# Kernel tuning notes

Measured on AMD Instinct MI355X. Metric: run time of the kernel, lower is better.

The kernel has to match this reference:

```python
import jax, jax.numpy as jnp
import numpy as np

N_NODES = 500000


def _gconv(x, src, dst, ew, w_neigh, b, w_self):
    # DGL GraphConv(norm='none'): multiply weight first (in>=out here), then aggregate.
    h = x @ w_neigh                      # [N, out]
    msg = h[src] * ew[:, None]           # [E, out]
    agg = jax.ops.segment_sum(msg, dst, num_segments=N_NODES)
    return agg + b + x @ w_self          # neigh conv (+bias) + self-loop linear (no bias)


def setup_inputs() -> dict:
    key = jax.random.key(0)
    ks = jax.random.split(key, 16)
    N, E, G, F = N_NODES, 16000000, 64, 16
    inp = {
        "x": jax.random.normal(ks[0], (N, F), jnp.float32),
        "src": jax.random.randint(ks[1], (E,), 0, N),
        "dst": jax.random.randint(ks[2], (E,), 0, N),
        "graph_id": jnp.sort(jax.random.randint(ks[3], (N,), 0, G)),
        "edge_weight": jax.random.uniform(ks[4], (E,), jnp.float32),
        "num_graphs": G,
        "w_neigh0": jax.random.normal(ks[5], (F, 1), jnp.float32),
        "b0": jax.random.normal(ks[6], (1,), jnp.float32),
        "w_self0": jax.random.normal(ks[7], (F, 1), jnp.float32),
        "w_neigh1": jax.random.normal(ks[8], (1, 1), jnp.float32),
        "b1": jax.random.normal(ks[9], (1,), jnp.float32),
        "w_self1": jax.random.normal(ks[10], (1, 1), jnp.float32),
        "w_neigh2": jax.random.normal(ks[11], (1, 1), jnp.float32),
        "b2": jax.random.normal(ks[12], (1,), jnp.float32),
        "w_self2": jax.random.normal(ks[13], (1, 1), jnp.float32),
        "fc1_w": jax.random.normal(ks[14], (8, 1), jnp.float32),
        "fc1_b": jax.random.normal(ks[15], (8,), jnp.float32),
        "out_w": jax.random.normal(jax.random.fold_in(key, 100), (4, 8), jnp.float32),
        "out_b": jax.random.normal(jax.random.fold_in(key, 101), (4,), jnp.float32),
    }
    return inp


def reference(x, src, dst, graph_id, edge_weight, num_graphs,
              w_neigh0, b0, w_self0, w_neigh1, b1, w_self1,
              w_neigh2, b2, w_self2, fc1_w, fc1_b, out_w, out_b):
    h = jax.nn.relu(_gconv(x, src, dst, edge_weight, w_neigh0, b0, w_self0))
    h = jax.nn.relu(_gconv(h, src, dst, edge_weight, w_neigh1, b1, w_self1))
    h = jax.nn.relu(_gconv(h, src, dst, edge_weight, w_neigh2, b2, w_self2))
    # dgl.sum_nodes: per-graph segment sum over batched graph -> [G, 1]
    hg = jax.ops.segment_sum(h, graph_id, num_segments=num_graphs)
    hg2 = jax.nn.sigmoid((hg @ fc1_w.T + fc1_b) * 1000.0)   # [G, 8]
    out = jax.nn.relu(hg2 @ out_w.T + out_b)                # [G, 4]
    return jax.nn.log_softmax(out, axis=1)
```

## Files before the change

### kernel.cpp

```cpp
#include <hip/hip_runtime.h>

#define N_NODES 500000
#define NGRAPH  64
#define FDIM    16
#define NB1     62
#define NPB1    8192
#define SH1     13
#define SLC     8
#define NBLK    1024
#define CH      4096
typedef unsigned int u32;
typedef unsigned long long u64;

__global__ __launch_bounds__(1024) void proj_hist(const int* __restrict__ dst, int E, int chunk,
                                                  u32* __restrict__ blockHist,
                                                  const float* __restrict__ x,
                                                  const float* __restrict__ wn,
                                                  const float* __restrict__ wsf,
                                                  float* __restrict__ a,
                                                  float* __restrict__ s) {
    __shared__ u32 cnt[NB1];
    if (blockIdx.x < NBLK) {
        if (threadIdx.x < NB1) cnt[threadIdx.x] = 0;
        __syncthreads();
        int b = blockIdx.x;
        int lo = b * chunk, hi = min(lo + chunk, E);
        int m = (hi - lo) & ~3;
        for (int i = lo + threadIdx.x * 4; i < lo + m; i += 4096) {
            int4 d = *(const int4*)(dst + i);
            atomicAdd(&cnt[((u32)d.x) >> SH1], 1u);
            atomicAdd(&cnt[((u32)d.y) >> SH1], 1u);
            atomicAdd(&cnt[((u32)d.z) >> SH1], 1u);
            atomicAdd(&cnt[((u32)d.w) >> SH1], 1u);
        }
        for (int i = lo + m + threadIdx.x; i < hi; i += 1024)
            atomicAdd(&cnt[((u32)dst[i]) >> SH1], 1u);
        __syncthreads();
        if (threadIdx.x < NB1)
            blockHist[(size_t)b * NB1 + threadIdx.x] = cnt[threadIdx.x];
    } else {
        int i = (blockIdx.x - NBLK) * 1024 + threadIdx.x;
        if (i >= N_NODES) return;
        const float4* xr = (const float4*)(x + (size_t)i * FDIM);
        float4 v0 = xr[0], v1 = xr[1], v2 = xr[2], v3 = xr[3];
        const float4* n4 = (const float4*)wn;
        const float4* s4 = (const float4*)wsf;
        float4 n0 = n4[0], n1 = n4[1], n2 = n4[2], n3 = n4[3];
        float4 w0 = s4[0], w1 = s4[1], w2 = s4[2], w3 = s4[3];
        float an = v0.x*n0.x + v0.y*n0.y + v0.z*n0.z + v0.w*n0.w
                 + v1.x*n1.x + v1.y*n1.y + v1.z*n1.z + v1.w*n1.w
                 + v2.x*n2.x + v2.y*n2.y + v2.z*n2.z + v2.w*n2.w
                 + v3.x*n3.x + v3.y*n3.y + v3.z*n3.z + v3.w*n3.w;
        float as = v0.x*w0.x + v0.y*w0.y + v0.z*w0.z + v0.w*w0.w
                 + v1.x*w1.x + v1.y*w1.y + v1.z*w1.z + v1.w*w1.w
                 + v2.x*w2.x + v2.y*w2.y + v2.z*w2.z + v2.w*w2.w
                 + v3.x*w3.x + v3.y*w3.y + v3.z*w3.z + v3.w*w3.w;
        a[i] = an;
        s[i] = as;
    }
}

__global__ __launch_bounds__(NBLK) void scan1_kernel(u32* __restrict__ blockHist,
                                                     u32* __restrict__ binTotal) {
    int j = blockIdx.x;
    __shared__ u32 lsum[NBLK];
    int t = threadIdx.x;
    u32 v = blockHist[(size_t)t * NB1 + j];
    lsum[t] = v;
    __syncthreads();
    u32 x = v;
    for (int off = 1; off < NBLK; off <<= 1) {
        u32 y = (t >= off) ? lsum[t - off] : 0u;
        __syncthreads();
        x += y; lsum[t] = x;
        __syncthreads();
    }
    if (t == NBLK - 1) binTotal[j] = x;
    blockHist[(size_t)t * NB1 + j] = x - v;
}

__global__ void scan2_kernel(const u32* __restrict__ binTotal, u32* __restrict__ binStart) {
    __shared__ u32 sh[64];
    int t = threadIdx.x;
    u32 v = (t < NB1) ? binTotal[t] : 0u;
    sh[t] = v;
    __syncthreads();
    for (int d = 1; d < 64; d <<= 1) {
        u32 y = (t >= d) ? sh[t - d] : 0u;
        __syncthreads();
        sh[t] += y;
        __syncthreads();
    }
    if (t < NB1) binStart[t] = sh[t] - v;
    if (t == 63) binStart[NB1] = sh[63];
}

__global__ __launch_bounds__(512) void scatter_staged(const int* __restrict__ src,
                                                      const int* __restrict__ dst,
                                                      const float* __restrict__ ew,
                                                      int E, int chunk,
                                                      const u32* __restrict__ blockHist,
                                                      const u32* __restrict__ binStart,
                                                      u64* __restrict__ binned) {
    __shared__ u32 cursor[64];
    __shared__ u32 cnt[64];
    __shared__ u32 off[64];
    __shared__ u64 stage[CH];
    __shared__ unsigned char binOf[CH];
    int b = blockIdx.x, tid = threadIdx.x;
    if (tid < NB1) cursor[tid] = binStart[tid] + blockHist[(size_t)b * NB1 + tid];
    int lo = b * chunk, hiB = min(lo + chunk, E);
    for (int base = lo; base < hiB; base += CH) {
        int n = min(CH, hiB - base);
        if (tid < 64) cnt[tid] = 0;
        __syncthreads();
        u32 rec[8]; float wv[8]; u32 bi[8], rk[8];
#pragma unroll
        for (int k = 0; k < 8; ++k) {
            int idx = base + k * 512 + tid;
            bi[k] = 0xFFFFFFFFu;
            if (idx < base + n) {
                u32 d  = (u32)dst[idx];
                bi[k]  = d >> SH1;
                rec[k] = ((u32)src[idx]) | ((d & (NPB1 - 1)) << 19);
                wv[k]  = ew[idx];
                rk[k]  = atomicAdd(&cnt[bi[k]], 1u);
            }
        }
        __syncthreads();
        if (tid < 64) off[tid] = cnt[tid];
        __syncthreads();
        for (int d2 = 1; d2 < 64; d2 <<= 1) {
            u32 y = 0;
            if (tid < 64 && tid >= d2) y = off[tid - d2];
            __syncthreads();
            if (tid < 64) off[tid] += y;
            __syncthreads();
        }
        if (tid < 64) off[tid] -= cnt[tid];
        __syncthreads();
#pragma unroll
        for (int k = 0; k < 8; ++k) {
            if (bi[k] != 0xFFFFFFFFu) {
                u32 p = off[bi[k]] + rk[k];
                stage[p] = (u64)rec[k] | ((u64)__float_as_uint(wv[k]) << 32);
                binOf[p] = (unsigned char)bi[k];
            }
        }
        __syncthreads();
        for (int p = tid; p < n; p += 512) {
            u32 jj = binOf[p];
            binned[cursor[jj] + ((u32)p - off[jj])] = stage[p];
        }
        __syncthreads();
        if (tid < NB1) cursor[tid] += cnt[tid];
        __syncthreads();
    }
}

__global__ __launch_bounds__(512) void bin_pass(const u64* __restrict__ binned,
                                                const u32* __restrict__ binStart,
                                                const float* __restrict__ hsrc,
                                                float* __restrict__ partials) {
    __shared__ float acc[NPB1];
    int j = blockIdx.x / SLC, sl = blockIdx.x % SLC;
    for (int t = threadIdx.x; t < NPB1; t += 512) acc[t] = 0.0f;
    __syncthreads();
    u32 blo = binStart[j], bhi = binStart[j + 1];
    u32 cj = bhi - blo;
    u32 per = (cj + SLC - 1) / SLC;
    u32 lo = blo + sl * per;
    u32 hi = min(lo + per, bhi);
    u32 i = lo + threadIdx.x;
    for (; i + 7u * 512u < hi; i += 8u * 512u) {
        u64 e[8];
#pragma unroll
        for (int k = 0; k < 8; ++k) e[k] = __builtin_nontemporal_load(&binned[i + (u32)k * 512u]);
        float g[8];
#pragma unroll
        for (int k = 0; k < 8; ++k) g[k] = hsrc[((u32)e[k]) & 0x7FFFFu];
#pragma unroll
        for (int k = 0; k < 8; ++k)
            atomicAdd(&acc[((u32)e[k]) >> 19], g[k] * __uint_as_float((u32)(e[k] >> 32)));
    }
    for (; i < hi; i += 512) {
        u64 e = __builtin_nontemporal_load(&binned[i]);
        atomicAdd(&acc[((u32)e) >> 19], hsrc[((u32)e) & 0x7FFFFu] * __uint_as_float((u32)(e >> 32)));
    }
    __syncthreads();
    float* p = partials + ((size_t)j * SLC + sl) * NPB1;
    for (int t = threadIdx.x; t < NPB1; t += 512)
        __builtin_nontemporal_store(acc[t], &p[t]);
}

template<bool LAST>
__global__ __launch_bounds__(256) void merge_update(const float* __restrict__ partials,
                                                    const float* __restrict__ selfv,
                                                    const float* __restrict__ wnp,
                                                    const float* __restrict__ bp,
                                                    const float* __restrict__ wsp,
                                                    float* __restrict__ hout,
                                                    const int* __restrict__ gid,
                                                    float* __restrict__ hg) {
    int n = blockIdx.x * blockDim.x + threadIdx.x;
    if (n >= N_NODES) return;
    int j = n >> SH1;
    int l = n & (NPB1 - 1);
    const float* p = partials + ((size_t)j * SLC) * NPB1 + l;
    float sum = 0.0f;
#pragma unroll
    for (int k = 0; k < SLC; ++k) sum += __builtin_nontemporal_load(&p[k * NPB1]);
    float scale = wnp ? wnp[0] : 1.0f;
    float wself = wsp ? wsp[0] : 1.0f;
    float v = fmaxf(sum * scale + bp[0] + selfv[n] * wself, 0.0f);
    hout[n] = v;
    if (LAST) {
        int g = gid[n];
        unsigned long long act = __ballot(1);
        int g0 = __shfl(g, 0);
        if (act == ~0ull && __all(g == g0)) {
            float t = v;
#pragma unroll
            for (int o = 32; o > 0; o >>= 1) t += __shfl_down(t, o);
            if ((threadIdx.x & 63) == 0) atomicAdd(&hg[g0], t);
        } else {
            atomicAdd(&hg[g], v);
        }
    }
}

__global__ void edge_pass(const int* __restrict__ src, const int* __restrict__ dst,
                          const float* __restrict__ ew, const float* __restrict__ h,
                          float* __restrict__ agg, const float* __restrict__ wnp, int E) {
    float scale = wnp ? wnp[0] : 1.0f;
    int stride = gridDim.x * blockDim.x;
    for (int i = blockIdx.x * blockDim.x + threadIdx.x; i < E; i += stride)
        atomicAdd(&agg[dst[i]], h[src[i]] * ew[i] * scale);
}
__global__ void node_update(const float* __restrict__ agg, const float* __restrict__ selfv,
                            const float* __restrict__ bp, const float* __restrict__ wsp,
                            float* __restrict__ hout) {
    int i = blockIdx.x * blockDim.x + threadIdx.x;
    if (i >= N_NODES) return;
    float wsc = wsp ? wsp[0] : 1.0f;
    hout[i] = fmaxf(agg[i] + bp[0] + selfv[i] * wsc, 0.0f);
}
__global__ void proj_kernel(const float* __restrict__ x, const float* __restrict__ wn,
                            const float* __restrict__ wsf, float* __restrict__ a,
                            float* __restrict__ s) {
    int i = blockIdx.x * blockDim.x + threadIdx.x;
    if (i >= N_NODES) return;
    float an = 0.f, as = 0.f;
    for (int k = 0; k < FDIM; ++k) {
        float v = x[(size_t)i * FDIM + k];
        an += v * wn[k]; as += v * wsf[k];
    }
    a[i] = an; s[i] = as;
}

__global__ __launch_bounds__(256) void graph_sum(const float* __restrict__ h,
                                                 const int* __restrict__ gid,
                                                 float* __restrict__ hg) {
    __shared__ float loc[NGRAPH];
    int t = threadIdx.x;
    if (t < NGRAPH) loc[t] = 0.0f;
    __syncthreads();
    int nq = N_NODES / 4;
    int stride = gridDim.x * blockDim.x;
    for (int q = blockIdx.x * blockDim.x + t; q < nq; q += stride) {
        int4   g4 = *(const int4*)(gid + 4 * q);
        float4 h4 = *(const float4*)(h + 4 * q);
        int g0 = __shfl(g4.x, 0);
        bool uni = (g4.x == g0) & (g4.w == g0);
        if (__all(uni)) {
            float v = h4.x + h4.y + h4.z + h4.w;
#pragma unroll
            for (int o = 32; o > 0; o >>= 1) v += __shfl_down(v, o);
            if ((t & 63) == 0) atomicAdd(&loc[g0], v);
        } else {
            atomicAdd(&loc[g4.x], h4.x);
            atomicAdd(&loc[g4.y], h4.y);
            atomicAdd(&loc[g4.z], h4.z);
            atomicAdd(&loc[g4.w], h4.w);
        }
    }
    __syncthreads();
    if (t < NGRAPH) atomicAdd(&hg[t], loc[t]);
}

__global__ void head_kernel(const float* __restrict__ hg,
                            const float* __restrict__ fc1w, const float* __restrict__ fc1b,
                            const float* __restrict__ outw, const float* __restrict__ outb,
                            float* __restrict__ out) {
    int g = threadIdx.x;
    if (g >= NGRAPH) return;
    float v = hg[g];
    float t[8];
#pragma unroll
    for (int j = 0; j < 8; ++j) {
        float z = (v * fc1w[j] + fc1b[j]) * 1000.0f;
        t[j] = 1.0f / (1.0f + expf(-z));
    }
    float o[4];
#pragma unroll
    for (int k = 0; k < 4; ++k) {
        float acc2 = outb[k];
#pragma unroll
        for (int j = 0; j < 8; ++j) acc2 += t[j] * outw[k * 8 + j];
        o[k] = fmaxf(acc2, 0.0f);
    }
    float m = fmaxf(fmaxf(o[0], o[1]), fmaxf(o[2], o[3]));
    float se = 0.0f;
#pragma unroll
    for (int k = 0; k < 4; ++k) se += expf(o[k] - m);
    float lse = m + logf(se);
#pragma unroll
    for (int k = 0; k < 4; ++k) out[g * 4 + k] = o[k] - lse;
}

extern "C" void kernel_launch(void* const* d_in, const int* in_sizes, int n_in,
                              void* d_out, int out_size, void* d_ws, size_t ws_size,
                              hipStream_t stream) {
    const float* x    = (const float*)d_in[0];
    const int*   src  = (const int*)  d_in[1];
    const int*   dst  = (const int*)  d_in[2];
    const int*   gid  = (const int*)  d_in[3];
    const float* ew   = (const float*)d_in[4];
    const float* wn0  = (const float*)d_in[6];
    const float* b0   = (const float*)d_in[7];
    const float* ws0  = (const float*)d_in[8];
    const float* wn1  = (const float*)d_in[9];
    const float* b1   = (const float*)d_in[10];
    const float* ws1  = (const float*)d_in[11];
    const float* wn2  = (const float*)d_in[12];
    const float* b2   = (const float*)d_in[13];
    const float* ws2  = (const float*)d_in[14];
    const float* fc1w = (const float*)d_in[15];
    const float* fc1b = (const float*)d_in[16];
    const float* outw = (const float*)d_in[17];
    const float* outb = (const float*)d_in[18];
    int E = in_sizes[1];

    const int BLK = 256;
    int nodeGrid = (N_NODES + BLK - 1) / BLK;
    char* ws = (char*)d_ws;

    size_t off = 0;
    u64* binned     = (u64*)(ws + off); off += (size_t)E * 8;
    u32* blockHist  = (u32*)(ws + off); off += (size_t)NBLK * NB1 * 4;
    u32* binStart   = (u32*)(ws + off); off += (NB1 + 2) * 4;
    off = (off + 63) & ~(size_t)63;
    u32* binTotal   = (u32*)(ws + off); off += (NB1 + 2) * 4;
    off = (off + 63) & ~(size_t)63;
    float* partials = (float*)(ws + off); off += (size_t)NB1 * SLC * NPB1 * 4;
    float* a  = (float*)(ws + off); off += (size_t)N_NODES * 4;
    float* s  = (float*)(ws + off); off += (size_t)N_NODES * 4;
    float* hg = (float*)(ws + off); off += 256;
    size_t need = off;

    if (ws_size >= need) {
        int chunk = (((E + NBLK - 1) / NBLK) + 3) & ~3;
        int projBlocks = (N_NODES + 1023) / 1024;

        proj_hist<<<NBLK + projBlocks, 1024, 0, stream>>>(dst, E, chunk, blockHist,
                                                          x, wn0, ws0, a, s);
        scan1_kernel<<<NB1, NBLK, 0, stream>>>(blockHist, binTotal);
        scan2_kernel<<<1, 64, 0, stream>>>(binTotal, binStart);
        scatter_staged<<<NBLK, 512, 0, stream>>>(src, dst, ew, E, chunk, blockHist,
                                                 binStart, binned);
        (void)hipMemsetAsync(hg, 0, NGRAPH * sizeof(float), stream);

        bin_pass<<<NB1 * SLC, 512, 0, stream>>>(binned, binStart, a, partials);
        merge_update<false><<<nodeGrid, BLK, 0, stream>>>(partials, s, nullptr, b0, nullptr,
                                                          s, gid, hg);
        bin_pass<<<NB1 * SLC, 512, 0, stream>>>(binned, binStart, s, partials);
        merge_update<false><<<nodeGrid, BLK, 0, stream>>>(partials, s, wn1, b1, ws1,
                                                          s, gid, hg);
        bin_pass<<<NB1 * SLC, 512, 0, stream>>>(binned, binStart, s, partials);
        merge_update<true><<<nodeGrid, BLK, 0, stream>>>(partials, s, wn2, b2, ws2,
                                                         s, gid, hg);

        head_kernel<<<1, 64, 0, stream>>>(hg, fc1w, fc1b, outw, outb, (float*)d_out);
    } else {
        float* wsb  = (float*)d_ws;
        float* fa   = wsb;
        float* fs   = wsb + 1 * (size_t)N_NODES;
        float* fagg = wsb + 2 * (size_t)N_NODES;
        float* fh   = wsb + 3 * (size_t)N_NODES;
        float* fhg  = wsb + 4 * (size_t)N_NODES;

        proj_kernel<<<nodeGrid, BLK, 0, stream>>>(x, wn0, ws0, fa, fs);

        (void)hipMemsetAsync(fagg, 0, (size_t)N_NODES * sizeof(float), stream);
        edge_pass<<<4096, BLK, 0, stream>>>(src, dst, ew, fa, fagg, nullptr, E);
        node_update<<<nodeGrid, BLK, 0, stream>>>(fagg, fs, b0, nullptr, fh);

        (void)hipMemsetAsync(fagg, 0, (size_t)N_NODES * sizeof(float), stream);
        edge_pass<<<4096, BLK, 0, stream>>>(src, dst, ew, fh, fagg, wn1, E);
        node_update<<<nodeGrid, BLK, 0, stream>>>(fagg, fh, b1, ws1, fh);

        (void)hipMemsetAsync(fagg, 0, (size_t)N_NODES * sizeof(float), stream);
        edge_pass<<<4096, BLK, 0, stream>>>(src, dst, ew, fh, fagg, wn2, E);
        node_update<<<nodeGrid, BLK, 0, stream>>>(fagg, fh, b2, ws2, fh);

        (void)hipMemsetAsync(fhg, 0, NGRAPH * sizeof(float), stream);
        graph_sum<<<512, 256, 0, stream>>>(fh, gid, fhg);
        head_kernel<<<1, 64, 0, stream>>>(fhg, fc1w, fc1b, outw, outb, (float*)d_out);
    }
}
```

Measured before the change: 467.0 us.

## Replicate histogram counters, enlarge scatter chunk, vectorize merge, use unsafe float atomics

Several independent tweaks. The histogram kernel gets eight replicated shared-memory counter sets to reduce LDS atomic contention. The scatter stage doubles its chunk to 8192 edges with 16 records per thread, which enlarges the shared staging buffer and register use. merge_update now handles four nodes per thread with float4 loads, and float atomicAdd calls are replaced by unsafeAtomicAdd so they can lower to hardware float atomics. The larger staging buffer (64KB for u64 plus binOf) may lower occupancy or exceed the LDS limit.

```diff
diff --git a/kernel.cpp b/kernel.cpp
--- a/kernel.cpp
+++ b/kernel.cpp
@@ -8,7 +8,7 @@
 #define SH1     13
 #define SLC     8
 #define NBLK    1024
-#define CH      4096
+#define CH      8192
 typedef unsigned int u32;
 typedef unsigned long long u64;
 
@@ -19,25 +19,31 @@
                                                   const float* __restrict__ wsf,
                                                   float* __restrict__ a,
                                                   float* __restrict__ s) {
-    __shared__ u32 cnt[NB1];
+    __shared__ u32 cnt[8][64];
     if (blockIdx.x < NBLK) {
-        if (threadIdx.x < NB1) cnt[threadIdx.x] = 0;
-        __syncthreads();
+        int tid = threadIdx.x;
+        for (int t = tid; t < 8 * 64; t += 1024) ((u32*)cnt)[t] = 0;
+        __syncthreads();
+        int rep = (tid >> 6) & 7;
         int b = blockIdx.x;
         int lo = b * chunk, hi = min(lo + chunk, E);
         int m = (hi - lo) & ~3;
-        for (int i = lo + threadIdx.x * 4; i < lo + m; i += 4096) {
+        for (int i = lo + tid * 4; i < lo + m; i += 4096) {
             int4 d = *(const int4*)(dst + i);
-            atomicAdd(&cnt[((u32)d.x) >> SH1], 1u);
-            atomicAdd(&cnt[((u32)d.y) >> SH1], 1u);
-            atomicAdd(&cnt[((u32)d.z) >> SH1], 1u);
-            atomicAdd(&cnt[((u32)d.w) >> SH1], 1u);
-        }
-        for (int i = lo + m + threadIdx.x; i < hi; i += 1024)
-            atomicAdd(&cnt[((u32)dst[i]) >> SH1], 1u);
-        __syncthreads();
-        if (threadIdx.x < NB1)
-            blockHist[(size_t)b * NB1 + threadIdx.x] = cnt[threadIdx.x];
+            atomicAdd(&cnt[rep][((u32)d.x) >> SH1], 1u);
+            atomicAdd(&cnt[rep][((u32)d.y) >> SH1], 1u);
+            atomicAdd(&cnt[rep][((u32)d.z) >> SH1], 1u);
+            atomicAdd(&cnt[rep][((u32)d.w) >> SH1], 1u);
+        }
+        for (int i = lo + m + tid; i < hi; i += 1024)
+            atomicAdd(&cnt[rep][((u32)dst[i]) >> SH1], 1u);
+        __syncthreads();
+        if (tid < NB1) {
+            u32 tot = 0;
+#pragma unroll
+            for (int r = 0; r < 8; ++r) tot += cnt[r][tid];
+            blockHist[(size_t)b * NB1 + tid] = tot;
+        }
     } else {
         int i = (blockIdx.x - NBLK) * 1024 + threadIdx.x;
         if (i >= N_NODES) return;
@@ -114,9 +120,9 @@
         int n = min(CH, hiB - base);
         if (tid < 64) cnt[tid] = 0;
         __syncthreads();
-        u32 rec[8]; float wv[8]; u32 bi[8], rk[8];
-#pragma unroll
-        for (int k = 0; k < 8; ++k) {
+        u32 rec[16]; float wv[16]; u32 bi[16], rk[16];
+#pragma unroll
+        for (int k = 0; k < 16; ++k) {
             int idx = base + k * 512 + tid;
             bi[k] = 0xFFFFFFFFu;
             if (idx < base + n) {
@@ -140,7 +146,7 @@
         if (tid < 64) off[tid] -= cnt[tid];
         __syncthreads();
 #pragma unroll
-        for (int k = 0; k < 8; ++k) {
+        for (int k = 0; k < 16; ++k) {
             if (bi[k] != 0xFFFFFFFFu) {
                 u32 p = off[bi[k]] + rk[k];
                 stage[p] = (u64)rec[k] | ((u64)__float_as_uint(wv[k]) << 32);
@@ -181,11 +187,12 @@
         for (int k = 0; k < 8; ++k) g[k] = hsrc[((u32)e[k]) & 0x7FFFFu];
 #pragma unroll
         for (int k = 0; k < 8; ++k)
-            atomicAdd(&acc[((u32)e[k]) >> 19], g[k] * __uint_as_float((u32)(e[k] >> 32)));
+            unsafeAtomicAdd(&acc[((u32)e[k]) >> 19], g[k] * __uint_as_float((u32)(e[k] >> 32)));
     }
     for (; i < hi; i += 512) {
         u64 e = __builtin_nontemporal_load(&binned[i]);
-        atomicAdd(&acc[((u32)e) >> 19], hsrc[((u32)e) & 0x7FFFFu] * __uint_as_float((u32)(e >> 32)));
+        unsafeAtomicAdd(&acc[((u32)e) >> 19],
+                        hsrc[((u32)e) & 0x7FFFFu] * __uint_as_float((u32)(e >> 32)));
     }
     __syncthreads();
     float* p = partials + ((size_t)j * SLC + sl) * NPB1;
@@ -202,29 +209,43 @@
                                                     float* __restrict__ hout,
                                                     const int* __restrict__ gid,
                                                     float* __restrict__ hg) {
-    int n = blockIdx.x * blockDim.x + threadIdx.x;
+    int q = blockIdx.x * blockDim.x + threadIdx.x;
+    int n = q * 4;
     if (n >= N_NODES) return;
     int j = n >> SH1;
     int l = n & (NPB1 - 1);
     const float* p = partials + ((size_t)j * SLC) * NPB1 + l;
-    float sum = 0.0f;
-#pragma unroll
-    for (int k = 0; k < SLC; ++k) sum += __builtin_nontemporal_load(&p[k * NPB1]);
+    float4 sum = make_float4(0.f, 0.f, 0.f, 0.f);
+#pragma unroll
+    for (int k = 0; k < SLC; ++k) {
+        float4 v = *(const float4*)(p + k * NPB1);
+        sum.x += v.x; sum.y += v.y; sum.z += v.z; sum.w += v.w;
+    }
     float scale = wnp ? wnp[0] : 1.0f;
+    float bias  = bp[0];
     float wself = wsp ? wsp[0] : 1.0f;
-    float v = fmaxf(sum * scale + bp[0] + selfv[n] * wself, 0.0f);
-    hout[n] = v;
+    float4 sv = *(const float4*)(selfv + n);
+    float4 o;
+    o.x = fmaxf(sum.x * scale + bias + sv.x * wself, 0.0f);
+    o.y = fmaxf(sum.y * scale + bias + sv.y * wself, 0.0f);
+    o.z = fmaxf(sum.z * scale + bias + sv.z * wself, 0.0f);
+    o.w = fmaxf(sum.w * scale + bias + sv.w * wself, 0.0f);
+    *(float4*)(hout + n) = o;
     if (LAST) {
-        int g = gid[n];
+        int4 g4 = *(const int4*)(gid + n);
         unsigned long long act = __ballot(1);
-        int g0 = __shfl(g, 0);
-        if (act == ~0ull && __all(g == g0)) {
-            float t = v;
-#pragma unroll
-            for (int o = 32; o > 0; o >>= 1) t += __shfl_down(t, o);
-            if ((threadIdx.x & 63) == 0) atomicAdd(&hg[g0], t);
+        int g0 = __shfl(g4.x, 0);
+        bool uni = (g4.x == g0) & (g4.w == g0);
+        if (act == ~0ull && __all(uni)) {
+            float t = o.x + o.y + o.z + o.w;
+#pragma unroll
+            for (int d = 32; d > 0; d >>= 1) t += __shfl_down(t, d);
+            if ((threadIdx.x & 63) == 0) unsafeAtomicAdd(&hg[g0], t);
         } else {
-            atomicAdd(&hg[g], v);
+            unsafeAtomicAdd(&hg[g4.x], o.x);
+            unsafeAtomicAdd(&hg[g4.y], o.y);
+            unsafeAtomicAdd(&hg[g4.z], o.z);
+            unsafeAtomicAdd(&hg[g4.w], o.w);
         }
     }
 }
@@ -235,7 +256,7 @@
     float scale = wnp ? wnp[0] : 1.0f;
     int stride = gridDim.x * blockDim.x;
     for (int i = blockIdx.x * blockDim.x + threadIdx.x; i < E; i += stride)
-        atomicAdd(&agg[dst[i]], h[src[i]] * ew[i] * scale);
+        unsafeAtomicAdd(&agg[dst[i]], h[src[i]] * ew[i] * scale);
 }
 __global__ void node_update(const float* __restrict__ agg, const float* __restrict__ selfv,
                             const float* __restrict__ bp, const float* __restrict__ wsp,
@@ -276,16 +297,16 @@
             float v = h4.x + h4.y + h4.z + h4.w;
 #pragma unroll
             for (int o = 32; o > 0; o >>= 1) v += __shfl_down(v, o);
-            if ((t & 63) == 0) atomicAdd(&loc[g0], v);
+            if ((t & 63) == 0) unsafeAtomicAdd(&loc[g0], v);
         } else {
-            atomicAdd(&loc[g4.x], h4.x);
-            atomicAdd(&loc[g4.y], h4.y);
-            atomicAdd(&loc[g4.z], h4.z);
-            atomicAdd(&loc[g4.w], h4.w);
-        }
-    }
-    __syncthreads();
-    if (t < NGRAPH) atomicAdd(&hg[t], loc[t]);
+            unsafeAtomicAdd(&loc[g4.x], h4.x);
+            unsafeAtomicAdd(&loc[g4.y], h4.y);
+            unsafeAtomicAdd(&loc[g4.z], h4.z);
+            unsafeAtomicAdd(&loc[g4.w], h4.w);
+        }
+    }
+    __syncthreads();
+    if (t < NGRAPH) unsafeAtomicAdd(&hg[t], loc[t]);
 }
 
 __global__ void head_kernel(const float* __restrict__ hg,
@@ -342,7 +363,8 @@
     int E = in_sizes[1];
 
     const int BLK = 256;
-    int nodeGrid = (N_NODES + BLK - 1) / BLK;
+    int nodeGrid  = (N_NODES + BLK - 1) / BLK;
+    int quadGrid  = (N_NODES / 4 + BLK - 1) / BLK;
     char* ws = (char*)d_ws;
 
     size_t off = 0;
@@ -371,13 +393,13 @@
         (void)hipMemsetAsync(hg, 0, NGRAPH * sizeof(float), stream);
 
         bin_pass<<<NB1 * SLC, 512, 0, stream>>>(binned, binStart, a, partials);
-        merge_update<false><<<nodeGrid, BLK, 0, stream>>>(partials, s, nullptr, b0, nullptr,
+        merge_update<false><<<quadGrid, BLK, 0, stream>>>(partials, s, nullptr, b0, nullptr,
                                                           s, gid, hg);
         bin_pass<<<NB1 * SLC, 512, 0, stream>>>(binned, binStart, s, partials);
-        merge_update<false><<<nodeGrid, BLK, 0, stream>>>(partials, s, wn1, b1, ws1,
+        merge_update<false><<<quadGrid, BLK, 0, stream>>>(partials, s, wn1, b1, ws1,
                                                           s, gid, hg);
         bin_pass<<<NB1 * SLC, 512, 0, stream>>>(binned, binStart, s, partials);
-        merge_update<true><<<nodeGrid, BLK, 0, stream>>>(partials, s, wn2, b2, ws2,
+        merge_update<true><<<quadGrid, BLK, 0, stream>>>(partials, s, wn2, b2, ws2,
                                                          s, gid, hg);
 
         head_kernel<<<1, 64, 0, stream>>>(hg, fc1w, fc1b, outw, outb, (float*)d_out);
```

New measurement: 504.1 us. 1.08x slower.
